# Performance work log

Hardware: AMD Instinct MI355X
Metric: run time of the kernel (lower is better)

Reference implementation:

```python
import jax, jax.numpy as jnp
import numpy as np

FULL = 128      # full_size D
BLOCK = 16      # block_size
C = 28          # num_channels
T = FULL // BLOCK   # tiles per axis = 8
N_OCC = 154
SL = (8, 72)    # region slice (start, stop) used on every axis; unaligned to BLOCK


def setup_inputs() -> dict:
    key = jax.random.key(0)
    # Deterministic occupancy with exactly N_OCC occupied tiles.
    rng = np.random.default_rng(0)
    occ_flat = np.zeros(T * T * T, dtype=bool)
    occ_flat[rng.permutation(T * T * T)[:N_OCC]] = True
    occupancy = jnp.asarray(occ_flat.reshape(T, T, T))
    # Sparse tile parameters: torch init is randn(...)*0.001, stacked here
    # in occupancy-nonzero (row-major) order, matching occupied_positions.
    tiles = jax.random.normal(key, (N_OCC, 7, C, BLOCK, BLOCK, BLOCK), dtype=jnp.float32) * 0.001
    return {"tiles": tiles, "occupancy": occupancy}


def reference(tiles, occupancy):
    """Faithful vectorized extract_region(slices=(SL, SL, SL)).

    Gathers all occupied tiles overlapping the region onto an aligned dense
    canvas (zero where unoccupied == the F.pad + add accumulation), then
    slices out the requested unaligned window. Returns a (7, 1, C, sx, sy, sz)
    array: entry j equals result[SUBBAND_KEYS[j]] of the torch dict.
    """
    s0, s1 = SL
    sx = s1 - s0                                   # 64
    t_start = s0 // BLOCK                          # first tile index per axis
    t_end = (s1 - 1) // BLOCK + 1                  # one past last tile
    nt = t_end - t_start                           # 5 tiles per axis

    occ_flat = occupancy.reshape(-1)
    # Map tile grid position -> row in `tiles` (row-major nonzero order).
    tile_idx = jnp.cumsum(occ_flat.astype(jnp.int32)) - 1

    g = jnp.arange(t_start, t_end)
    # Linear grid indices of the nt x nt x nt tiles covering the region.
    lin = (g[:, None, None] * T + g[None, :, None]) * T + g[None, None, :]
    sel_occ = occ_flat[lin]                        # (nt, nt, nt) bool
    sel_idx = jnp.clip(tile_idx[lin], 0)           # safe gather index

    # Gather tiles; zero out unoccupied slots (they contribute nothing).
    gathered = tiles[sel_idx] * sel_occ[..., None, None, None, None, None].astype(tiles.dtype)
    # (gx, gy, gz, 7, C, bx, by, bz) -> (7, C, gx, bx, gy, by, gz, bz) -> dense canvas
    canvas = gathered.transpose(3, 4, 0, 5, 1, 6, 2, 7).reshape(
        7, C, nt * BLOCK, nt * BLOCK, nt * BLOCK)

    o = s0 - t_start * BLOCK                       # offset of region inside canvas
    region = canvas[:, :, o:o + sx, o:o + sx, o:o + sx]
    return region[:, None]                         # (7, 1, C, sx, sx, sx)
```

## Files before the change

kernel.cpp:

```cpp
#include <hip/hip_runtime.h>

#define S0 8

typedef float f4 __attribute__((ext_vector_type(4)));

__global__ void build_lut_kernel(const void* __restrict__ occ_raw,
                                 int* __restrict__ lut) {
    __shared__ int flag[512];
    __shared__ int psum[512];
    __shared__ int cnt8;
    const int t = threadIdx.x;
    const unsigned char* p8 = (const unsigned char*)occ_raw;
    if (t == 0) cnt8 = 0;
    __syncthreads();
    const unsigned char b = p8[t];
    unsigned long long m = __ballot(b != 0);
    if ((t & 63) == 0) atomicAdd(&cnt8, __popcll(m));
    __syncthreads();
    int o;
    if (cnt8 > 128) {
        o = (b != 0) ? 1 : 0;
    } else {
        o = (((const unsigned int*)occ_raw)[t] != 0u) ? 1 : 0;
    }
    flag[t] = o;
    psum[t] = o;
    __syncthreads();
    for (int off = 1; off < 512; off <<= 1) {
        int v = (t >= off) ? psum[t - off] : 0;
        __syncthreads();
        psum[t] += v;
        __syncthreads();
    }
    if (t < 125) {
        int gx = t / 25;
        int r  = t - gx * 25;
        int gy = r / 5;
        int gz = r - gy * 5;
        int lin = (gx * 8 + gy) * 8 + gz;
        lut[t] = flag[lin] ? (psum[lin] - 1) : -1;
    }
}

__global__ __launch_bounds__(256) void gather_kernel(
    const float* __restrict__ tiles, const int* __restrict__ lut,
    float* __restrict__ out, int half) {
    __shared__ int slut[125];
    if (threadIdx.x < 125) slut[threadIdx.x] = lut[threadIdx.x];
    __syncthreads();
    const int i0 = blockIdx.x * 256 + threadIdx.x;
#pragma unroll
    for (int u = 0; u < 2; ++u) {
        const int i = i0 + u * half;
        int zq = i & 15;
        int t1 = i >> 4;
        int y  = t1 & 63;
        int t2 = t1 >> 6;
        int x  = t2 & 63;
        int t3 = t2 >> 6;
        int j  = t3 / 28;
        int c  = t3 - j * 28;
        int Z = zq * 4 + S0;
        int Y = y + S0;
        int X = x + S0;
        int gz = Z >> 4, bz = Z & 15;
        int gy = Y >> 4, by = Y & 15;
        int gx = X >> 4, bx = X & 15;
        int tidx = slut[(gx * 5 + gy) * 5 + gz];
        f4 v = (f4)(0.0f);
        if (tidx >= 0) {
            size_t src = (((size_t)tidx * 7 + (size_t)j) * 28 + (size_t)c) * 4096
                       + (size_t)(bx * 256 + by * 16 + bz);
            v = __builtin_nontemporal_load((const f4*)(tiles + src));
        }
        __builtin_nontemporal_store(v, (f4*)(out + (size_t)i * 4));
    }
}

extern "C" void kernel_launch(void* const* d_in, const int* in_sizes, int n_in,
                              void* d_out, int out_size, void* d_ws, size_t ws_size,
                              hipStream_t stream) {
    const float* tiles = (const float*)d_in[0];
    const void*  occ   = d_in[1];
    float* out = (float*)d_out;
    int* lut = (int*)d_ws;

    build_lut_kernel<<<1, 512, 0, stream>>>(occ, lut);

    int half = out_size / 8;
    int blocks = half / 256;
    gather_kernel<<<blocks, 256, 0, stream>>>(tiles, lut, out, half);
}
```

Before: 604.0 us.

## Assign half a z-row per thread with per-tile segment loads

Each thread now produces 32 contiguous output floats, half of a 64-wide z row, instead of two scattered float4s. It does three LUT lookups per thread rather than one per float4 and issues up to eight float4 loads and stores per thread. The nontemporal load and store builtins are dropped in favour of plain accesses. The change cuts index arithmetic and LUT traffic and raises per-thread memory-level parallelism, but each thread's accesses are strided across lanes, which may hurt coalescing, and cache behaviour changes.

```diff
diff --git a/kernel.cpp b/kernel.cpp
--- a/kernel.cpp
+++ b/kernel.cpp
@@ -44,37 +44,48 @@
 
 __global__ __launch_bounds__(256) void gather_kernel(
     const float* __restrict__ tiles, const int* __restrict__ lut,
-    float* __restrict__ out, int half) {
+    float* __restrict__ out) {
     __shared__ int slut[125];
     if (threadIdx.x < 125) slut[threadIdx.x] = lut[threadIdx.x];
     __syncthreads();
-    const int i0 = blockIdx.x * 256 + threadIdx.x;
-#pragma unroll
-    for (int u = 0; u < 2; ++u) {
-        const int i = i0 + u * half;
-        int zq = i & 15;
-        int t1 = i >> 4;
-        int y  = t1 & 63;
-        int t2 = t1 >> 6;
-        int x  = t2 & 63;
-        int t3 = t2 >> 6;
-        int j  = t3 / 28;
-        int c  = t3 - j * 28;
-        int Z = zq * 4 + S0;
-        int Y = y + S0;
-        int X = x + S0;
-        int gz = Z >> 4, bz = Z & 15;
-        int gy = Y >> 4, by = Y & 15;
-        int gx = X >> 4, bx = X & 15;
-        int tidx = slut[(gx * 5 + gy) * 5 + gz];
-        f4 v = (f4)(0.0f);
-        if (tidx >= 0) {
-            size_t src = (((size_t)tidx * 7 + (size_t)j) * 28 + (size_t)c) * 4096
-                       + (size_t)(bx * 256 + by * 16 + bz);
-            v = __builtin_nontemporal_load((const f4*)(tiles + src));
-        }
-        __builtin_nontemporal_store(v, (f4*)(out + (size_t)i * 4));
+
+    const int t   = blockIdx.x * 256 + threadIdx.x;
+    const int g   = t & 1;
+    const int row = t >> 1;
+    const int y   = row & 63;
+    const int x   = (row >> 6) & 63;
+    const int t3  = row >> 12;
+
+    const int Y = y + S0, X = x + S0;
+    const int gx = X >> 4, bx = X & 15;
+    const int gy = Y >> 4, by = Y & 15;
+
+    const int lb = (gx * 5 + gy) * 5 + 2 * g;
+    const int tA = slut[lb];
+    const int tB = slut[lb + 1];
+    const int tC = slut[lb + 2];
+
+    const size_t inner = (size_t)(bx * 256 + by * 16);
+
+    f4 v0, v1, v2, v3, v4, v5, v6, v7;
+    v0 = v1 = v2 = v3 = v4 = v5 = v6 = v7 = (f4)(0.0f);
+
+    if (tA >= 0) {
+        const f4* p = (const f4*)(tiles + ((size_t)tA * 196 + t3) * 4096 + inner + 8);
+        v0 = p[0]; v1 = p[1];
     }
+    if (tB >= 0) {
+        const f4* p = (const f4*)(tiles + ((size_t)tB * 196 + t3) * 4096 + inner);
+        v2 = p[0]; v3 = p[1]; v4 = p[2]; v5 = p[3];
+    }
+    if (tC >= 0) {
+        const f4* p = (const f4*)(tiles + ((size_t)tC * 196 + t3) * 4096 + inner);
+        v6 = p[0]; v7 = p[1];
+    }
+
+    f4* q = (f4*)(out + (size_t)row * 64 + 32 * g);
+    q[0] = v0; q[1] = v1; q[2] = v2; q[3] = v3;
+    q[4] = v4; q[5] = v5; q[6] = v6; q[7] = v7;
 }
 
 extern "C" void kernel_launch(void* const* d_in, const int* in_sizes, int n_in,
@@ -87,7 +98,6 @@
 
     build_lut_kernel<<<1, 512, 0, stream>>>(occ, lut);
 
-    int half = out_size / 8;
-    int blocks = half / 256;
-    gather_kernel<<<blocks, 256, 0, stream>>>(tiles, lut, out, half);
+    int blocks = out_size / 8192;
+    gather_kernel<<<blocks, 256, 0, stream>>>(tiles, lut, out);
 }
```

New measurement: 622.6 us. 1.03x slower.

## Fuse LUT build into gather kernel with ballot-based prefix counts

Applied to the files above, without the earlier changes.

Removes the separate single-block LUT kernel and has every gather block compute the 125-entry tile index table itself, using wave ballots and popcounts instead of a shared-memory scan. Each thread now handles 8 float4 elements instead of 2, and the j/c split is folded into one flat index. Nontemporal loads and stores are replaced with ordinary ones. This saves a kernel launch and the workspace round-trip, but every block now redoes the occupancy reads and bit counting, and far fewer blocks are launched.

```diff
diff --git a/kernel.cpp b/kernel.cpp
--- a/kernel.cpp
+++ b/kernel.cpp
@@ -4,76 +4,75 @@
 
 typedef float f4 __attribute__((ext_vector_type(4)));
 
-__global__ void build_lut_kernel(const void* __restrict__ occ_raw,
-                                 int* __restrict__ lut) {
-    __shared__ int flag[512];
-    __shared__ int psum[512];
+__global__ __launch_bounds__(256) void gather_kernel(
+    const float* __restrict__ tiles, const void* __restrict__ occ_raw,
+    float* __restrict__ out, int eighth ) {
+    __shared__ unsigned long long mw[8];
+    __shared__ int slut[125];
     __shared__ int cnt8;
+
     const int t = threadIdx.x;
-    const unsigned char* p8 = (const unsigned char*)occ_raw;
+    const unsigned char* p8  = (const unsigned char*)occ_raw;
+    const unsigned int*  p32 = (const unsigned int*)occ_raw;
+
     if (t == 0) cnt8 = 0;
     __syncthreads();
-    const unsigned char b = p8[t];
-    unsigned long long m = __ballot(b != 0);
-    if ((t & 63) == 0) atomicAdd(&cnt8, __popcll(m));
+    {
+        unsigned long long m0 = __ballot(p8[t] != 0);
+        unsigned long long m1 = __ballot(p8[t + 256] != 0);
+        if ((t & 63) == 0) atomicAdd(&cnt8, __popcll(m0) + __popcll(m1));
+    }
     __syncthreads();
-    int o;
-    if (cnt8 > 128) {
-        o = (b != 0) ? 1 : 0;
-    } else {
-        o = (((const unsigned int*)occ_raw)[t] != 0u) ? 1 : 0;
+    const bool bytelay = (cnt8 > 128);
+    {
+        bool o0 = bytelay ? (p8[t] != 0)       : (p32[t] != 0u);
+        bool o1 = bytelay ? (p8[t + 256] != 0) : (p32[t + 256] != 0u);
+        unsigned long long m0 = __ballot(o0);
+        unsigned long long m1 = __ballot(o1);
+        int w = t >> 6;
+        if ((t & 63) == 0) { mw[w] = m0; mw[w + 4] = m1; }
     }
-    flag[t] = o;
-    psum[t] = o;
     __syncthreads();
-    for (int off = 1; off < 512; off <<= 1) {
-        int v = (t >= off) ? psum[t - off] : 0;
-        __syncthreads();
-        psum[t] += v;
-        __syncthreads();
-    }
     if (t < 125) {
         int gx = t / 25;
         int r  = t - gx * 25;
         int gy = r / 5;
         int gz = r - gy * 5;
         int lin = (gx * 8 + gy) * 8 + gz;
-        lut[t] = flag[lin] ? (psum[lin] - 1) : -1;
+        int wi = lin >> 6, bi = lin & 63;
+        unsigned long long cur = mw[wi];
+        int occ_here = (int)((cur >> bi) & 1ull);
+        int s = 0;
+        for (int w = 0; w < wi; ++w) s += __popcll(mw[w]);
+        unsigned long long lowmask =
+            (bi == 63) ? ~0ull : ((1ull << (bi + 1)) - 1ull);
+        s += __popcll(cur & lowmask);
+        slut[t] = occ_here ? (s - 1) : -1;
     }
-}
+    __syncthreads();
 
-__global__ __launch_bounds__(256) void gather_kernel(
-    const float* __restrict__ tiles, const int* __restrict__ lut,
-    float* __restrict__ out, int half) {
-    __shared__ int slut[125];
-    if (threadIdx.x < 125) slut[threadIdx.x] = lut[threadIdx.x];
-    __syncthreads();
-    const int i0 = blockIdx.x * 256 + threadIdx.x;
+    const int i0 = blockIdx.x * 256 + t;
 #pragma unroll
-    for (int u = 0; u < 2; ++u) {
-        const int i = i0 + u * half;
-        int zq = i & 15;
-        int t1 = i >> 4;
-        int y  = t1 & 63;
-        int t2 = t1 >> 6;
-        int x  = t2 & 63;
-        int t3 = t2 >> 6;
-        int j  = t3 / 28;
-        int c  = t3 - j * 28;
-        int Z = zq * 4 + S0;
-        int Y = y + S0;
-        int X = x + S0;
-        int gz = Z >> 4, bz = Z & 15;
-        int gy = Y >> 4, by = Y & 15;
-        int gx = X >> 4, bx = X & 15;
-        int tidx = slut[(gx * 5 + gy) * 5 + gz];
+    for (int u = 0; u < 8; ++u) {
+        const int i  = i0 + u * eighth;
+        const int zq = i & 15;
+        const int y  = (i >> 4) & 63;
+        const int x  = (i >> 10) & 63;
+        const int t3 = i >> 16;
+        const int Z = zq * 4 + S0;
+        const int Y = y + S0;
+        const int X = x + S0;
+        const int gz = Z >> 4, bz = Z & 15;
+        const int gy = Y >> 4, by = Y & 15;
+        const int gx = X >> 4, bx = X & 15;
+        const int tidx = slut[(gx * 5 + gy) * 5 + gz];
         f4 v = (f4)(0.0f);
         if (tidx >= 0) {
-            size_t src = (((size_t)tidx * 7 + (size_t)j) * 28 + (size_t)c) * 4096
+            size_t src = ((size_t)tidx * 196 + (size_t)t3) * 4096
                        + (size_t)(bx * 256 + by * 16 + bz);
-            v = __builtin_nontemporal_load((const f4*)(tiles + src));
+            v = *(const f4*)(tiles + src);
         }
-        __builtin_nontemporal_store(v, (f4*)(out + (size_t)i * 4));
+        *(f4*)(out + (size_t)i * 4) = v;
     }
 }
 
@@ -83,11 +82,10 @@
     const float* tiles = (const float*)d_in[0];
     const void*  occ   = d_in[1];
     float* out = (float*)d_out;
-    int* lut = (int*)d_ws;
+    (void)d_ws; (void)ws_size;
 
-    build_lut_kernel<<<1, 512, 0, stream>>>(occ, lut);
-
-    int half = out_size / 8;
-    int blocks = half / 256;
-    gather_kernel<<<blocks, 256, 0, stream>>>(tiles, lut, out, half);
+    int n4     = out_size / 4;
+    int eighth = n4 / 8;
+    int blocks = eighth / 256;
+    gather_kernel<<<blocks, 256, 0, stream>>>(tiles, occ, out, eighth);
 }
```

Result: no change. 615.6 us (+1.9%).
